# Kernel optimization log

Hardware: AMD Instinct MI355X
Metric: run time of the kernel (lower is better)

Reference implementation:

```python
import jax, jax.numpy as jnp
import numpy as np

EPS = 1e-5
B, S, P = 2, 512, 4096
TD, SD, H, ED = 512, 384, 8, 32
HD = TD // H


def _ln(x, g, b):
    m = jnp.mean(x, axis=-1, keepdims=True)
    v = jnp.var(x, axis=-1, keepdims=True)
    return (x - m) * jax.lax.rsqrt(v + EPS) * g + b


def setup_inputs() -> dict:
    key = jax.random.key(0)
    ks = iter(jax.random.split(key, 24))

    def lin(din, dout):
        W = jax.random.normal(next(ks), (din, dout), jnp.float32) / np.sqrt(din)
        b = jnp.zeros((dout,), jnp.float32)
        return W, b

    Wq, bq = lin(TD, TD)
    Wk, bk = lin(SD, TD)
    Wv, bv = lin(SD, TD)
    Wo, bo = lin(TD, TD)
    W1, b1 = lin(TD, 4 * TD)
    W2, b2 = lin(4 * TD, TD)
    edge_emb = jax.random.normal(next(ks), (H, ED), jnp.float32)
    ep_w = jax.random.normal(next(ks), (ED,), jnp.float32) / np.sqrt(ED)
    ep_b = jnp.zeros((), jnp.float32)

    return dict(
        text_features=jax.random.normal(next(ks), (B, S, TD), jnp.float32),
        shape_features=jax.random.normal(next(ks), (B, P, SD), jnp.float32),
        tn_g=jnp.ones((TD,), jnp.float32), tn_b=jnp.zeros((TD,), jnp.float32),
        sn_g=jnp.ones((SD,), jnp.float32), sn_b=jnp.zeros((SD,), jnp.float32),
        Wq=Wq, bq=bq, Wk=Wk, bk=bk, Wv=Wv, bv=bv,
        edge_emb=edge_emb, ep_w=ep_w, ep_b=ep_b,
        Wo=Wo, bo=bo,
        on_g=jnp.ones((TD,), jnp.float32), on_b=jnp.zeros((TD,), jnp.float32),
        W1=W1, b1=b1, W2=W2, b2=b2,
        fn_g=jnp.ones((TD,), jnp.float32), fn_b=jnp.zeros((TD,), jnp.float32),
    )


def reference(text_features, shape_features, tn_g, tn_b, sn_g, sn_b,
              Wq, bq, Wk, bk, Wv, bv, edge_emb, ep_w, ep_b, Wo, bo,
              on_g, on_b, W1, b1, W2, b2, fn_g, fn_b):
    b, n, _ = text_features.shape
    tn = _ln(text_features, tn_g, tn_b)
    sn = _ln(shape_features, sn_g, sn_b)
    residual = text_features

    # [b, h, n, d] projections
    q = (tn @ Wq + bq).reshape(b, n, H, HD).transpose(0, 2, 1, 3)
    k = (sn @ Wk + bk).reshape(b, -1, H, HD).transpose(0, 2, 1, 3)
    v = (sn @ Wv + bv).reshape(b, -1, H, HD).transpose(0, 2, 1, 3)

    scale = HD ** -0.5
    base_attn = jnp.einsum('bhid,bhjd->bhij', q, k) * scale  # [b,h,n,p]

    # edge_attn[:,h] = base_attn[:,h,:,:,None] * edge_emb[h]; then Linear(ED,1)+LeakyReLU.
    # Algebraically: score = leaky_relu(base_attn * (edge_emb @ ep_w) + ep_b)
    s = edge_emb @ ep_w  # [H] per-head scalar
    edge_scores = jax.nn.leaky_relu(base_attn * s[None, :, None, None] + ep_b, 0.2)

    attn = jax.nn.softmax(base_attn + edge_scores, axis=-1)
    out = jnp.einsum('bhij,bhjd->bhid', attn, v)
    out = out.transpose(0, 2, 1, 3).reshape(b, n, TD)
    out = out @ Wo + bo
    out = _ln(residual + out, on_g, on_b)

    ffn = jax.nn.gelu(out @ W1 + b1, approximate=False) @ W2 + b2
    out = _ln(out + ffn, fn_g, fn_b)
    return out, attn
```

## Files before the change

kernel.cpp:

```cpp
#include <hip/hip_runtime.h>
#include <math.h>

#define B_  2
#define S_  512
#define P_  4096
#define TD_ 512
#define SD_ 384
#define H_  8
#define HD_ 64
#define FF_ 2048

typedef _Float16 half8 __attribute__((ext_vector_type(8)));
typedef _Float16 half4 __attribute__((ext_vector_type(4)));
typedef float floatx4 __attribute__((ext_vector_type(4)));

__device__ __forceinline__ half8 f4x2_to_h8(float4 a, float4 b) {
    half8 r;
    r[0] = (_Float16)a.x; r[1] = (_Float16)a.y; r[2] = (_Float16)a.z; r[3] = (_Float16)a.w;
    r[4] = (_Float16)b.x; r[5] = (_Float16)b.y; r[6] = (_Float16)b.z; r[7] = (_Float16)b.w;
    return r;
}

__device__ __forceinline__ float2 block_sum2(float a, float b) {
    for (int off = 32; off > 0; off >>= 1) {
        a += __shfl_down(a, off);
        b += __shfl_down(b, off);
    }
    __shared__ float sa[8], sb[8];
    int w = threadIdx.x >> 6;
    if ((threadIdx.x & 63) == 0) { sa[w] = a; sb[w] = b; }
    __syncthreads();
    int nw = blockDim.x >> 6;
    float ta = 0.f, tb = 0.f;
    for (int i = 0; i < nw; ++i) { ta += sa[i]; tb += sb[i]; }
    __syncthreads();
    return make_float2(ta, tb);
}

__global__ __launch_bounds__(256) void prep_kernel(
    const float* __restrict__ s0p, const float* __restrict__ s1p,
    const float* __restrict__ s2p, const float* __restrict__ s3p,
    const float* __restrict__ s4p, const float* __restrict__ s5p,
    _Float16* __restrict__ d0p, _Float16* __restrict__ d1p,
    _Float16* __restrict__ d2p, _Float16* __restrict__ d3p,
    _Float16* __restrict__ d4p, _Float16* __restrict__ d5p,
    const float* __restrict__ text, const float* __restrict__ shape,
    const float* __restrict__ tn_g, const float* __restrict__ tn_b,
    const float* __restrict__ sn_g, const float* __restrict__ sn_b,
    _Float16* __restrict__ tn_h, _Float16* __restrict__ sn_h,
    float* __restrict__ ctx_zero)
{
    __shared__ float ts[32][33];
    int id = blockIdx.x;
    int tid = threadIdx.x;
    if (id < 2944) {
        const float* src; _Float16* dst; int K, N, t, nlog;
        if (id < 256)       { src=s0p; dst=d0p; K=512;  N=512;  t=id;       nlog=4; }
        else if (id < 448)  { src=s1p; dst=d1p; K=384;  N=512;  t=id-256;   nlog=4; }
        else if (id < 640)  { src=s2p; dst=d2p; K=384;  N=512;  t=id-448;   nlog=4; }
        else if (id < 896)  { src=s3p; dst=d3p; K=512;  N=512;  t=id-640;   nlog=4; }
        else if (id < 1920) { src=s4p; dst=d4p; K=512;  N=2048; t=id-896;   nlog=6; }
        else                { src=s5p; dst=d5p; K=2048; N=512;  t=id-1920;  nlog=4; }
        int n0 = (t & ((1 << nlog) - 1)) << 5;
        int k0 = (t >> nlog) << 5;
#pragma unroll
        for (int i = 0; i < 4; ++i) {
            int e = i * 256 + tid;
            int kk = e >> 5, nn = e & 31;
            ts[kk][nn] = src[(size_t)(k0 + kk) * N + n0 + nn];
        }
        __syncthreads();
#pragma unroll
        for (int i = 0; i < 4; ++i) {
            int e = i * 256 + tid;
            int nn = e >> 5, kk = e & 31;
            dst[(size_t)(n0 + nn) * K + k0 + kk] = (_Float16)ts[kk][nn];
        }
        return;
    }
    if (id >= 12160) {
        int i = (id - 12160) * 256 + tid;
        ((float4*)ctx_zero)[i] = make_float4(0.f, 0.f, 0.f, 0.f);
        return;
    }
    int row = id - 2944;
    const float* xr; const float* g; const float* be; _Float16* yr; int D;
    if (row < 1024) {
        D = 512; xr = text + (size_t)row * 512; g = tn_g; be = tn_b;
        yr = tn_h + (size_t)row * 512;
    } else {
        int r2 = row - 1024;
        D = 384; xr = shape + (size_t)r2 * 384; g = sn_g; be = sn_b;
        yr = sn_h + (size_t)r2 * 384;
    }
    float s = 0.f, s2 = 0.f;
    for (int i = tid; i < D; i += 256) {
        float v = xr[i]; s += v; s2 += v * v;
    }
    float2 r = block_sum2(s, s2);
    float mean = r.x / (float)D;
    float var  = r.y / (float)D - mean * mean;
    float rstd = rsqrtf(var + 1e-5f);
    for (int i = tid; i < D; i += 256)
        yr[i] = (_Float16)((xr[i] - mean) * rstd * g[i] + be[i]);
}

__global__ __launch_bounds__(256) void ln_add_kernel(
    const float* __restrict__ a, const float* __restrict__ c, int np, int cstride,
    const float* __restrict__ g, const float* __restrict__ be,
    float* __restrict__ yf, _Float16* __restrict__ yh)
{
    int row = blockIdx.x;
    int i0 = threadIdx.x, i1 = threadIdx.x + 256;
    const float* ar = a + (size_t)row * 512;
    const float* cr = c + (size_t)row * 512;
    float v0 = ar[i0], v1 = ar[i1];
    for (int t = 0; t < np; ++t) {
        v0 += cr[(size_t)t * cstride + i0];
        v1 += cr[(size_t)t * cstride + i1];
    }
    float2 rd = block_sum2(v0 + v1, v0 * v0 + v1 * v1);
    float mean = rd.x / 512.f;
    float var  = rd.y / 512.f - mean * mean;
    float rstd = rsqrtf(var + 1e-5f);
    float o0 = (v0 - mean) * rstd * g[i0] + be[i0];
    float o1 = (v1 - mean) * rstd * g[i1] + be[i1];
    if (yf) { yf[(size_t)row * 512 + i0] = o0; yf[(size_t)row * 512 + i1] = o1; }
    if (yh) { yh[(size_t)row * 512 + i0] = (_Float16)o0; yh[(size_t)row * 512 + i1] = (_Float16)o1; }
}

template<int ACT, int OUTF, int OUTH, int SPLITK, int AF32>
__global__ __launch_bounds__(256) void gemm_f16_kernel(
    const _Float16* __restrict__ A, const _Float16* __restrict__ Bt,
    const float* __restrict__ bias, float* __restrict__ Cf,
    _Float16* __restrict__ Ch, int M, int N, int K)
{
    __shared__ _Float16 As[128 * 40];
    __shared__ _Float16 Bs[128 * 40];
    int tid = threadIdx.x;
    int bm = blockIdx.y * 128, bn = blockIdx.x * 128;
    int wave = tid >> 6, lane = tid & 63, quad = lane >> 4, r = lane & 15;
    int mh = (wave & 1) * 64, nh = (wave >> 1) * 64;

    floatx4 acc[4][4];
    floatx4 zz = {0.f, 0.f, 0.f, 0.f};
#pragma unroll
    for (int i = 0; i < 4; ++i)
#pragma unroll
        for (int j = 0; j < 4; ++j) acc[i][j] = zz;

    int srow = tid >> 2;
    int sko  = (tid & 3) * 8;

    int ksplit = (SPLITK > 1) ? blockIdx.z : 0;
    int kbeg = ksplit * (K / SPLITK);
    int kend = kbeg + K / SPLITK;

    const float*    Af  = (const float*)A;
    const _Float16* Ap0 = A  + (size_t)(bm + srow) * K + sko;
    const _Float16* Ap1 = A  + (size_t)(bm + srow + 64) * K + sko;
    const float*    Af0 = Af + (size_t)(bm + srow) * K + sko;
    const float*    Af1 = Af + (size_t)(bm + srow + 64) * K + sko;
    const _Float16* Bp0 = Bt + (size_t)(bn + srow) * K + sko;
    const _Float16* Bp1 = Bt + (size_t)(bn + srow + 64) * K + sko;

    half8 ra0, ra1;
    float4 fa0l, fa0h, fa1l, fa1h;
    if (AF32) {
        fa0l = *(const float4*)(Af0 + kbeg); fa0h = *(const float4*)(Af0 + kbeg + 4);
        fa1l = *(const float4*)(Af1 + kbeg); fa1h = *(const float4*)(Af1 + kbeg + 4);
    } else {
        ra0 = *(const half8*)(Ap0 + kbeg);
        ra1 = *(const half8*)(Ap1 + kbeg);
    }
    half8 rb0 = *(const half8*)(Bp0 + kbeg);
    half8 rb1 = *(const half8*)(Bp1 + kbeg);

    for (int k0 = kbeg; k0 < kend; k0 += 32) {
        if (AF32) {
            *(half8*)&As[srow * 40 + sko]        = f4x2_to_h8(fa0l, fa0h);
            *(half8*)&As[(srow + 64) * 40 + sko] = f4x2_to_h8(fa1l, fa1h);
        } else {
            *(half8*)&As[srow * 40 + sko]        = ra0;
            *(half8*)&As[(srow + 64) * 40 + sko] = ra1;
        }
        *(half8*)&Bs[srow * 40 + sko]        = rb0;
        *(half8*)&Bs[(srow + 64) * 40 + sko] = rb1;
        __syncthreads();
        if (k0 + 32 < kend) {
            if (AF32) {
                fa0l = *(const float4*)(Af0 + k0 + 32); fa0h = *(const float4*)(Af0 + k0 + 36);
                fa1l = *(const float4*)(Af1 + k0 + 32); fa1h = *(const float4*)(Af1 + k0 + 36);
            } else {
                ra0 = *(const half8*)(Ap0 + k0 + 32);
                ra1 = *(const half8*)(Ap1 + k0 + 32);
            }
            rb0 = *(const half8*)(Bp0 + k0 + 32);
            rb1 = *(const half8*)(Bp1 + k0 + 32);
        }
        half8 af[4], bf[4];
#pragma unroll
        for (int t = 0; t < 4; ++t) {
            af[t] = *(const half8*)&As[(mh + t * 16 + r) * 40 + quad * 8];
            bf[t] = *(const half8*)&Bs[(nh + t * 16 + r) * 40 + quad * 8];
        }
#pragma unroll
        for (int i = 0; i < 4; ++i)
#pragma unroll
            for (int j = 0; j < 4; ++j)
                acc[i][j] = __builtin_amdgcn_mfma_f32_16x16x32_f16(af[i], bf[j], acc[i][j], 0, 0, 0);
        __syncthreads();
    }

#pragma unroll
    for (int j = 0; j < 4; ++j) {
        int col = bn + nh + j * 16 + r;
        float bv = (SPLITK == 1 || ksplit == 0) ? bias[col] : 0.f;
#pragma unroll
        for (int i = 0; i < 4; ++i) {
#pragma unroll
            for (int g = 0; g < 4; ++g) {
                int row = bm + mh + i * 16 + quad * 4 + g;
                float v = acc[i][j][g] + bv;
                if (ACT) v = 0.5f * v * (1.0f + erff(v * 0.70710678118654752f));
                if (OUTF) Cf[(size_t)ksplit * M * N + (size_t)row * N + col] = v;
                if (OUTH) Ch[(size_t)row * N + col] = (_Float16)v;
            }
        }
    }
}

__global__ __launch_bounds__(512) void qkv_gemm_kernel(
    const _Float16* __restrict__ tn, const _Float16* __restrict__ sn,
    const _Float16* __restrict__ Wqt, const _Float16* __restrict__ Wkt,
    const _Float16* __restrict__ Wvt,
    const float* __restrict__ bq, const float* __restrict__ bk,
    const float* __restrict__ bv,
    _Float16* __restrict__ Qh, _Float16* __restrict__ Kh, _Float16* __restrict__ Vth)
{
    __shared__ _Float16 As[256 * 40];
    __shared__ _Float16 Bs[128 * 40];
    int by = blockIdx.y;
    const _Float16* A; const _Float16* Bt; const float* bias; _Float16* out;
    int K, bm, vt;
    if (by < 4)       { A = tn; Bt = Wqt; bias = bq; K = 512; bm = by * 256;        vt = 0; out = Qh;  }
    else if (by < 36) { A = sn; Bt = Wkt; bias = bk; K = 384; bm = (by - 4) * 256;  vt = 0; out = Kh;  }
    else              { A = sn; Bt = Wvt; bias = bv; K = 384; bm = (by - 36) * 256; vt = 1; out = Vth; }
    int bn = blockIdx.x * 128;
    int tid = threadIdx.x;
    int wave = tid >> 6, lane = tid & 63, quad = lane >> 4, r = lane & 15;
    int mh = (wave >> 1) * 64, nh = (wave & 1) * 64;

    floatx4 acc[4][4];
    floatx4 zz = {0.f, 0.f, 0.f, 0.f};
#pragma unroll
    for (int i = 0; i < 4; ++i)
#pragma unroll
        for (int j = 0; j < 4; ++j) acc[i][j] = zz;

    int arow = tid >> 2, ako = (tid & 3) * 8;
    const _Float16* ApA0 = A  + (size_t)(bm + arow) * K + ako;
    const _Float16* ApA1 = A  + (size_t)(bm + arow + 128) * K + ako;
    const _Float16* BpB  = Bt + (size_t)(bn + arow) * K + ako;

    half8 ra0 = *(const half8*)(ApA0);
    half8 ra1 = *(const half8*)(ApA1);
    half8 rb  = *(const half8*)(BpB);

    for (int k0 = 0; k0 < K; k0 += 32) {
        *(half8*)&As[arow * 40 + ako]         = ra0;
        *(half8*)&As[(arow + 128) * 40 + ako] = ra1;
        *(half8*)&Bs[arow * 40 + ako]         = rb;
        __syncthreads();
        if (k0 + 32 < K) {
            ra0 = *(const half8*)(ApA0 + k0 + 32);
            ra1 = *(const half8*)(ApA1 + k0 + 32);
            rb  = *(const half8*)(BpB  + k0 + 32);
        }
        half8 af[4], bf[4];
#pragma unroll
        for (int t = 0; t < 4; ++t) {
            af[t] = *(const half8*)&As[(mh + t * 16 + r) * 40 + quad * 8];
            bf[t] = *(const half8*)&Bs[(nh + t * 16 + r) * 40 + quad * 8];
        }
#pragma unroll
        for (int i = 0; i < 4; ++i)
#pragma unroll
            for (int j = 0; j < 4; ++j)
                acc[i][j] = __builtin_amdgcn_mfma_f32_16x16x32_f16(af[i], bf[j], acc[i][j], 0, 0, 0);
        __syncthreads();
    }

#pragma unroll
    for (int j = 0; j < 4; ++j) {
        int col = bn + nh + j * 16 + r;
        float bvv = bias[col];
#pragma unroll
        for (int i = 0; i < 4; ++i) {
#pragma unroll
            for (int g = 0; g < 4; ++g) {
                int row = bm + mh + i * 16 + quad * 4 + g;
                float v = acc[i][j][g] + bvv;
                if (!vt) {
                    out[(size_t)row * 512 + col] = (_Float16)v;
                } else {
                    int bb = row >> 12, pp = row & 4095;
                    int hh = col >> 6,  dd = col & 63;
                    out[((size_t)((bb * 8 + hh) * 64 + dd)) * 4096 + pp] = (_Float16)v;
                }
            }
        }
    }
}

__global__ __launch_bounds__(256) void score_stats_kernel(
    const _Float16* __restrict__ Qh, const _Float16* __restrict__ Kh,
    const float* __restrict__ edge_emb, const float* __restrict__ ep_w,
    const float* __restrict__ ep_b, float2* __restrict__ part)
{
    __shared__ _Float16 Qs[128 * 72];
    __shared__ _Float16 Ks[128 * 72];
    __shared__ float mred[2][128];
    __shared__ float sred[2][128];
    int bid = blockIdx.x;
    int slot = bid & 7, idx = bid >> 3;
    int g4 = slot + 8 * (idx >> 2);
    int s0 = (idx & 3) * 128;
    int p0 = (g4 & 31) * 128;
    int bh = g4 >> 5, h = bh & 7, b = bh >> 3;
    int tid = threadIdx.x;
    int wave = tid >> 6, lane = tid & 63, quad = lane >> 4, r = lane & 15;
    int mh = (wave & 1) * 64, nh = (wave >> 1) * 64;

#pragma unroll
    for (int i = 0; i < 4; ++i) {
        int row = i * 32 + (tid >> 3);
        int ko  = (tid & 7) * 8;
        *(half8*)&Qs[row * 72 + ko] = *(const half8*)(Qh + (size_t)(b * S_ + s0 + row) * TD_ + h * HD_ + ko);
        *(half8*)&Ks[row * 72 + ko] = *(const half8*)(Kh + (size_t)(b * P_ + p0 + row) * TD_ + h * HD_ + ko);
    }
    float s_h = 0.f;
#pragma unroll
    for (int e = 0; e < 32; ++e) s_h += edge_emb[h * 32 + e] * ep_w[e];
    float epbv = ep_b[0];
    __syncthreads();

    floatx4 acc[4][4];
    floatx4 zz = {0.f, 0.f, 0.f, 0.f};
#pragma unroll
    for (int i = 0; i < 4; ++i)
#pragma unroll
        for (int j = 0; j < 4; ++j) acc[i][j] = zz;

#pragma unroll
    for (int c = 0; c < 2; ++c) {
        half8 af[4], bf[4];
#pragma unroll
        for (int t = 0; t < 4; ++t) {
            af[t] = *(const half8*)&Qs[(mh + t * 16 + r) * 72 + c * 32 + quad * 8];
            bf[t] = *(const half8*)&Ks[(nh + t * 16 + r) * 72 + c * 32 + quad * 8];
        }
#pragma unroll
        for (int i = 0; i < 4; ++i)
#pragma unroll
            for (int j = 0; j < 4; ++j)
                acc[i][j] = __builtin_amdgcn_mfma_f32_16x16x32_f16(af[i], bf[j], acc[i][j], 0, 0, 0);
    }

    const float scale = 0.125f;
#pragma unroll
    for (int i = 0; i < 4; ++i)
#pragma unroll
        for (int j = 0; j < 4; ++j)
#pragma unroll
            for (int g = 0; g < 4; ++g) {
                float base = acc[i][j][g] * scale;
                float t = fmaf(base, s_h, epbv);
                float e = (t >= 0.f) ? t : 0.2f * t;
                acc[i][j][g] = base + e;
            }

    float mv[16], sv[16];
#pragma unroll
    for (int i = 0; i < 4; ++i)
#pragma unroll
        for (int g = 0; g < 4; ++g)
            mv[i * 4 + g] = fmaxf(fmaxf(acc[i][0][g], acc[i][1][g]),
                                  fmaxf(acc[i][2][g], acc[i][3][g]));
#pragma unroll
    for (int mask = 1; mask <= 8; mask <<= 1)
#pragma unroll
        for (int t = 0; t < 16; ++t)
            mv[t] = fmaxf(mv[t], __shfl_xor(mv[t], mask));
#pragma unroll
    for (int i = 0; i < 4; ++i)
#pragma unroll
        for (int g = 0; g < 4; ++g) {
            float s = 0.f;
#pragma unroll
            for (int j = 0; j < 4; ++j) s += __expf(acc[i][j][g] - mv[i * 4 + g]);
            sv[i * 4 + g] = s;
        }
#pragma unroll
    for (int mask = 1; mask <= 8; mask <<= 1)
#pragma unroll
        for (int t = 0; t < 16; ++t)
            sv[t] += __shfl_xor(sv[t], mask);

    if (r == 0) {
#pragma unroll
        for (int i = 0; i < 4; ++i)
#pragma unroll
            for (int g = 0; g < 4; ++g) {
                int row = mh + i * 16 + quad * 4 + g;
                mred[wave >> 1][row] = mv[i * 4 + g];
                sred[wave >> 1][row] = sv[i * 4 + g];
            }
    }
    __syncthreads();
    if (tid < 128) {
        float m0 = mred[0][tid], m1 = mred[1][tid];
        float m = fmaxf(m0, m1);
        float s = sred[0][tid] * __expf(m0 - m) + sred[1][tid] * __expf(m1 - m);
        part[(size_t)(p0 >> 7) * (B_ * H_ * S_) + (size_t)bh * S_ + s0 + tid] = make_float2(m, s);
    }
}

__global__ __launch_bounds__(256) void attn_pv_kernel(
    const _Float16* __restrict__ Qh, const _Float16* __restrict__ Kh,
    const _Float16* __restrict__ Vt,
    const float* __restrict__ edge_emb, const float* __restrict__ ep_w,
    const float* __restrict__ ep_b, const float2* __restrict__ part,
    float* __restrict__ attn, float* __restrict__ ctx_f32)
{
    __shared__ _Float16 Qs[32 * 72];
    __shared__ _Float16 Ks[128 * 72];
    __shared__ _Float16 Vs[64 * 136];
    __shared__ _Float16 As[32 * 136];
    __shared__ float2 ms_sh[32];

    int bid = blockIdx.x;
    int slot = bid & 7, idx = bid >> 3;
    int g16 = slot + 8 * (idx >> 4);
    int s0 = (idx & 15) * 32;
    int split = g16 & 7;
    int bh = g16 >> 3, h = bh & 7, b = bh >> 3;
    int tid = threadIdx.x;
    int wave = tid >> 6, lane = tid & 63, quad = lane >> 4, r = lane & 15;

    {
        int row = tid >> 3, ko = (tid & 7) * 8;
        *(half8*)&Qs[row * 72 + ko] =
            *(const half8*)(Qh + (size_t)(b * S_ + s0 + row) * TD_ + h * HD_ + ko);
    }
    if (tid < 32) {
        int base = bh * S_ + s0 + tid;
        float2 v = part[base];
        float m = v.x, l = v.y;
#pragma unroll
        for (int t = 1; t < 32; ++t) {
            float2 p = part[(size_t)t * (B_ * H_ * S_) + base];
            float nm = fmaxf(m, p.x);
            l = l * __expf(m - nm) + p.y * __expf(p.x - nm);
            m = nm;
        }
        ms_sh[tid] = make_float2(m, 1.0f / l);
    }

    float s_h = 0.f;
#pragma unroll
    for (int e = 0; e < 32; ++e) s_h += edge_emb[h * 32 + e] * ep_w[e];
    float epbv = ep_b[0];

    const _Float16* Kbase = Kh + (size_t)b * P_ * TD_ + h * HD_;
    const _Float16* Vbase = Vt + (size_t)bh * 64 * P_;

    int pg0 = split * 512;
    half8 rk[4], rv[4];
#pragma unroll
    for (int ii = 0; ii < 4; ++ii) {
        int e = ii * 256 + tid;
        rk[ii] = *(const half8*)(Kbase + (size_t)(pg0 + (e >> 3)) * TD_ + (e & 7) * 8);
        rv[ii] = *(const half8*)(Vbase + (size_t)(e >> 4) * P_ + pg0 + (e & 15) * 8);
    }

    floatx4 zz = {0.f, 0.f, 0.f, 0.f};
    floatx4 accpv[2];
    accpv[0] = zz; accpv[1] = zz;
    const float scale = 0.125f;

    for (int c = 0; c < 4; ++c) {
        int pg = pg0 + c * 128;
#pragma unroll
        for (int ii = 0; ii < 4; ++ii) {
            int e = ii * 256 + tid;
            *(half8*)&Ks[(e >> 3) * 72 + (e & 7) * 8]  = rk[ii];
            *(half8*)&Vs[(e >> 4) * 136 + (e & 15) * 8] = rv[ii];
        }
        __syncthreads();
        if (c < 3) {
            int pn = pg + 128;
#pragma unroll
            for (int ii = 0; ii < 4; ++ii) {
                int e = ii * 256 + tid;
                rk[ii] = *(const half8*)(Kbase + (size_t)(pn + (e >> 3)) * TD_ + (e & 7) * 8);
                rv[ii] = *(const half8*)(Vbase + (size_t)(e >> 4) * P_ + pn + (e & 15) * 8);
            }
        }

        floatx4 accs[2][2];
        accs[0][0] = zz; accs[0][1] = zz; accs[1][0] = zz; accs[1][1] = zz;
#pragma unroll
        for (int c2 = 0; c2 < 2; ++c2) {
            half8 aq[2], bk2[2];
#pragma unroll
            for (int i = 0; i < 2; ++i)
                aq[i] = *(const half8*)&Qs[(i * 16 + r) * 72 + c2 * 32 + quad * 8];
#pragma unroll
            for (int j = 0; j < 2; ++j)
                bk2[j] = *(const half8*)&Ks[(wave * 32 + j * 16 + r) * 72 + c2 * 32 + quad * 8];
#pragma unroll
            for (int i = 0; i < 2; ++i)
#pragma unroll
                for (int j = 0; j < 2; ++j)
                    accs[i][j] = __builtin_amdgcn_mfma_f32_16x16x32_f16(aq[i], bk2[j], accs[i][j], 0, 0, 0);
        }

#pragma unroll
        for (int i = 0; i < 2; ++i)
#pragma unroll
            for (int j = 0; j < 2; ++j) {
                int colp = wave * 32 + j * 16 + r;
#pragma unroll
                for (int g = 0; g < 4; ++g) {
                    int srow = i * 16 + quad * 4 + g;
                    float base = accs[i][j][g] * scale;
                    float t = fmaf(base, s_h, epbv);
                    float e = (t >= 0.f) ? t : 0.2f * t;
                    float z = base + e;
                    float2 ms = ms_sh[srow];
                    float p = __expf(z - ms.x) * ms.y;
                    As[srow * 136 + colp] = (_Float16)p;
                }
            }
        __syncthreads();

#pragma unroll
        for (int it = 0; it < 4; ++it) {
            int e = it * 256 + tid;
            int row = e >> 5, c4 = (e & 31) * 4;
            half4 hv = *(const half4*)&As[row * 136 + c4];
            floatx4 fv = { (float)hv[0], (float)hv[1], (float)hv[2], (float)hv[3] };
            __builtin_nontemporal_store(fv,
                (floatx4*)&attn[((size_t)bh * S_ + s0 + row) * P_ + pg + c4]);
        }

#pragma unroll
        for (int cc = 0; cc < 4; ++cc) {
            half8 bv = *(const half8*)&Vs[(wave * 16 + r) * 136 + cc * 32 + quad * 8];
#pragma unroll
            for (int i2 = 0; i2 < 2; ++i2) {
                half8 ap = *(const half8*)&As[(i2 * 16 + r) * 136 + cc * 32 + quad * 8];
                accpv[i2] = __builtin_amdgcn_mfma_f32_16x16x32_f16(ap, bv, accpv[i2], 0, 0, 0);
            }
        }
        __syncthreads();
    }

#pragma unroll
    for (int i2 = 0; i2 < 2; ++i2)
#pragma unroll
        for (int g = 0; g < 4; ++g) {
            int srow = s0 + i2 * 16 + quad * 4 + g;
            int d = wave * 16 + r;
            atomicAdd(&ctx_f32[(size_t)(b * S_ + srow) * TD_ + h * HD_ + d], accpv[i2][g]);
        }
}

extern "C" void kernel_launch(void* const* d_in, const int* in_sizes, int n_in,
                              void* d_out, int out_size, void* d_ws, size_t ws_size,
                              hipStream_t stream) {
    const float* text  = (const float*)d_in[0];
    const float* shape = (const float*)d_in[1];
    const float* tn_g  = (const float*)d_in[2];
    const float* tn_b  = (const float*)d_in[3];
    const float* sn_g  = (const float*)d_in[4];
    const float* sn_b  = (const float*)d_in[5];
    const float* Wq    = (const float*)d_in[6];
    const float* bq    = (const float*)d_in[7];
    const float* Wk    = (const float*)d_in[8];
    const float* bk    = (const float*)d_in[9];
    const float* Wv    = (const float*)d_in[10];
    const float* bv    = (const float*)d_in[11];
    const float* edge  = (const float*)d_in[12];
    const float* epw   = (const float*)d_in[13];
    const float* epb   = (const float*)d_in[14];
    const float* Wo    = (const float*)d_in[15];
    const float* bo    = (const float*)d_in[16];
    const float* on_g  = (const float*)d_in[17];
    const float* on_b  = (const float*)d_in[18];
    const float* W1    = (const float*)d_in[19];
    const float* b1    = (const float*)d_in[20];
    const float* W2    = (const float*)d_in[21];
    const float* b2    = (const float*)d_in[22];
    const float* fn_g  = (const float*)d_in[23];
    const float* fn_b  = (const float*)d_in[24];

    float* out_f  = (float*)d_out;
    float* attn_f = out_f + (size_t)B_ * S_ * TD_;

    char* w = (char*)d_ws;
    _Float16* tn_h   = (_Float16*)w; w += (size_t)1024 * 512 * 2;
    _Float16* sn_h   = (_Float16*)w; w += (size_t)8192 * 384 * 2;
    _Float16* Q_h    = (_Float16*)w; w += (size_t)1024 * 512 * 2;
    _Float16* K_h    = (_Float16*)w; w += (size_t)8192 * 512 * 2;
    _Float16* Vt_h   = (_Float16*)w; w += (size_t)16 * 64 * 4096 * 2;
    float*    ctx_f32 = (float*)w;   w += (size_t)1024 * 512 * 4;
    _Float16* out1_h = (_Float16*)w; w += (size_t)1024 * 512 * 2;
    _Float16* h1_h   = (_Float16*)w; w += (size_t)1024 * 2048 * 2;
    _Float16* Wqt    = (_Float16*)w; w += (size_t)512 * 512 * 2;
    _Float16* Wkt    = (_Float16*)w; w += (size_t)512 * 384 * 2;
    _Float16* Wvt    = (_Float16*)w; w += (size_t)512 * 384 * 2;
    _Float16* Wot    = (_Float16*)w; w += (size_t)512 * 512 * 2;
    _Float16* W1t    = (_Float16*)w; w += (size_t)2048 * 512 * 2;
    _Float16* W2t    = (_Float16*)w; w += (size_t)512 * 2048 * 2;
    float*    out1_f = (float*)w;    w += (size_t)1024 * 512 * 4;
    float*    ctx_part = (float*)w;  w += (size_t)4 * 1024 * 512 * 4;

    float2* part = (float2*)sn_h;

    prep_kernel<<<2944 + 1024 + 8192 + 512, 256, 0, stream>>>(
        Wq, Wk, Wv, Wo, W1, W2, Wqt, Wkt, Wvt, Wot, W1t, W2t,
        text, shape, tn_g, tn_b, sn_g, sn_b, tn_h, sn_h, ctx_f32);

    qkv_gemm_kernel<<<dim3(4, 68), 512, 0, stream>>>(tn_h, sn_h, Wqt, Wkt, Wvt,
                                                     bq, bk, bv, Q_h, K_h, Vt_h);

    score_stats_kernel<<<2048, 256, 0, stream>>>(Q_h, K_h, edge, epw, epb, part);
    attn_pv_kernel<<<2048, 256, 0, stream>>>(Q_h, K_h, Vt_h, edge, epw, epb, part, attn_f, ctx_f32);

    gemm_f16_kernel<0,1,0,4,1><<<dim3(4, 8, 4), 256, 0, stream>>>(
        (const _Float16*)ctx_f32, Wot, bo, ctx_part, nullptr, 1024, 512, 512);
    ln_add_kernel<<<B_ * S_, 256, 0, stream>>>(text, ctx_part, 4, 1024 * 512, on_g, on_b, out1_f, out1_h);

    gemm_f16_kernel<1,0,1,1,0><<<dim3(16, 8), 256, 0, stream>>>(out1_h, W1t, b1, nullptr, h1_h, 1024, 2048, 512);
    gemm_f16_kernel<0,1,0,4,0><<<dim3(4, 8, 4), 256, 0, stream>>>(h1_h, W2t, b2, ctx_part, nullptr, 1024, 512, 2048);
    ln_add_kernel<<<B_ * S_, 256, 0, stream>>>(out1_f, ctx_part, 4, 1024 * 512, fn_g, fn_b, out_f, nullptr);
}
```

Before: 335.2 us.

## Cache per-tile softmax numerators in fp16 buffer instead of recomputing QK scores

The stats pass now writes exp(score - tile max) as fp16 into a large workspace buffer, and a new PV kernel reads it back, rescales it by the combined softmax statistics, writes attn and does the PV MFMA. This drops the second QK^T recomputation in the attention kernel. The cost is an extra 64MB fp16 write and read. The path runs only if the workspace is large enough, otherwise the old recompute path is kept. Storing probabilities in fp16 before rescaling adds some precision loss to the attn output.

Result: slower. 366.5 us (+9.3%).

```diff
diff --git a/kernel.cpp b/kernel.cpp
--- a/kernel.cpp
+++ b/kernel.cpp
@@ -313,15 +313,20 @@
     }
 }
 
+template<int WP>
 __global__ __launch_bounds__(256) void score_stats_kernel(
     const _Float16* __restrict__ Qh, const _Float16* __restrict__ Kh,
     const float* __restrict__ edge_emb, const float* __restrict__ ep_w,
-    const float* __restrict__ ep_b, float2* __restrict__ part)
+    const float* __restrict__ ep_b, float2* __restrict__ part,
+    _Float16* __restrict__ Pbuf)
 {
-    __shared__ _Float16 Qs[128 * 72];
-    __shared__ _Float16 Ks[128 * 72];
+    __shared__ _Float16 smem[2 * 128 * 72];
     __shared__ float mred[2][128];
     __shared__ float sred[2][128];
+    _Float16* Qs = smem;
+    _Float16* Ks = smem + 128 * 72;
+    _Float16* Ps = smem;
+
     int bid = blockIdx.x;
     int slot = bid & 7, idx = bid >> 3;
     int g4 = slot + 8 * (idx >> 2);
@@ -398,7 +403,11 @@
         for (int g = 0; g < 4; ++g) {
             float s = 0.f;
 #pragma unroll
-            for (int j = 0; j < 4; ++j) s += __expf(acc[i][j][g] - mv[i * 4 + g]);
+            for (int j = 0; j < 4; ++j) {
+                float e = __expf(acc[i][j][g] - mv[i * 4 + g]);
+                acc[i][j][g] = e;
+                s += e;
+            }
             sv[i * 4 + g] = s;
         }
 #pragma unroll
@@ -418,15 +427,157 @@
             }
     }
     __syncthreads();
+
+    if (WP) {
+#pragma unroll
+        for (int i = 0; i < 4; ++i)
+#pragma unroll
+            for (int g = 0; g < 4; ++g) {
+                int row = mh + i * 16 + quad * 4 + g;
+                float mfull = fmaxf(mred[0][row], mred[1][row]);
+                float sc = __expf(mv[i * 4 + g] - mfull);
+#pragma unroll
+                for (int j = 0; j < 4; ++j)
+                    Ps[row * 136 + (nh + j * 16 + r)] = (_Float16)(acc[i][j][g] * sc);
+            }
+    }
+
     if (tid < 128) {
         float m0 = mred[0][tid], m1 = mred[1][tid];
         float m = fmaxf(m0, m1);
         float s = sred[0][tid] * __expf(m0 - m) + sred[1][tid] * __expf(m1 - m);
         part[(size_t)(p0 >> 7) * (B_ * H_ * S_) + (size_t)bh * S_ + s0 + tid] = make_float2(m, s);
     }
-}
-
-__global__ __launch_bounds__(256) void attn_pv_kernel(
+
+    if (WP) {
+        __syncthreads();
+#pragma unroll
+        for (int it = 0; it < 8; ++it) {
+            int e = it * 256 + tid;
+            int row = e >> 4, c8 = (e & 15) * 8;
+            half8 hv = *(const half8*)&Ps[row * 136 + c8];
+            __builtin_nontemporal_store(hv,
+                (half8*)(Pbuf + ((size_t)bh * S_ + s0 + row) * P_ + p0 + c8));
+        }
+    }
+}
+
+__global__ __launch_bounds__(256) void attn_pv_pc_kernel(
+    const _Float16* __restrict__ Pbuf, const _Float16* __restrict__ Vt,
+    const float2* __restrict__ part,
+    float* __restrict__ attn, float* __restrict__ ctx_f32)
+{
+    __shared__ _Float16 Vs[64 * 136];
+    __shared__ _Float16 As[32 * 136];
+    __shared__ float rs_sh[4][32];
+
+    int bid = blockIdx.x;
+    int slot = bid & 7, idx = bid >> 3;
+    int g16 = slot + 8 * (idx >> 4);
+    int s0 = (idx & 15) * 32;
+    int split = g16 & 7;
+    int bh = g16 >> 3, h = bh & 7, b = bh >> 3;
+    int tid = threadIdx.x;
+    int wave = tid >> 6, lane = tid & 63, quad = lane >> 4, r = lane & 15;
+
+    if (tid < 32) {
+        int base = bh * S_ + s0 + tid;
+        float2 v = part[base];
+        float m = v.x, l = v.y;
+#pragma unroll
+        for (int t = 1; t < 32; ++t) {
+            float2 p = part[(size_t)t * (B_ * H_ * S_) + base];
+            float nm = fmaxf(m, p.x);
+            l = l * __expf(m - nm) + p.y * __expf(p.x - nm);
+            m = nm;
+        }
+        float invl = 1.0f / l;
+#pragma unroll
+        for (int c = 0; c < 4; ++c) {
+            float mt = part[(size_t)(split * 4 + c) * (B_ * H_ * S_) + base].x;
+            rs_sh[c][tid] = __expf(mt - m) * invl;
+        }
+    }
+
+    const _Float16* Vbase = Vt + (size_t)bh * 64 * P_;
+    const _Float16* Pb    = Pbuf + ((size_t)bh * S_ + s0) * P_;
+    int pg0 = split * 512;
+    int prow = tid >> 4, ppo = (tid & 15) * 8;
+
+    half8 rv[4], rp0, rp1;
+#pragma unroll
+    for (int ii = 0; ii < 4; ++ii) {
+        int e = ii * 256 + tid;
+        rv[ii] = *(const half8*)(Vbase + (size_t)(e >> 4) * P_ + pg0 + (e & 15) * 8);
+    }
+    rp0 = *(const half8*)(Pb + (size_t)prow * P_ + pg0 + ppo);
+    rp1 = *(const half8*)(Pb + (size_t)(prow + 16) * P_ + pg0 + ppo);
+
+    floatx4 zz = {0.f, 0.f, 0.f, 0.f};
+    floatx4 accpv[2];
+    accpv[0] = zz; accpv[1] = zz;
+
+    __syncthreads();
+
+    for (int c = 0; c < 4; ++c) {
+        int pg = pg0 + c * 128;
+#pragma unroll
+        for (int ii = 0; ii < 4; ++ii) {
+            int e = ii * 256 + tid;
+            *(half8*)&Vs[(e >> 4) * 136 + (e & 15) * 8] = rv[ii];
+        }
+        float rs0 = rs_sh[c][prow], rs1 = rs_sh[c][prow + 16];
+        half8 a0, a1;
+        floatx4 f0a, f0b, f1a, f1b;
+#pragma unroll
+        for (int k = 0; k < 4; ++k) {
+            float u0 = (float)rp0[k]     * rs0; f0a[k] = u0; a0[k]     = (_Float16)u0;
+            float u1 = (float)rp0[k + 4] * rs0; f0b[k] = u1; a0[k + 4] = (_Float16)u1;
+            float w0 = (float)rp1[k]     * rs1; f1a[k] = w0; a1[k]     = (_Float16)w0;
+            float w1 = (float)rp1[k + 4] * rs1; f1b[k] = w1; a1[k + 4] = (_Float16)w1;
+        }
+        *(half8*)&As[prow * 136 + ppo]        = a0;
+        *(half8*)&As[(prow + 16) * 136 + ppo] = a1;
+        float* ar0 = &attn[((size_t)bh * S_ + s0 + prow) * P_ + pg + ppo];
+        float* ar1 = &attn[((size_t)bh * S_ + s0 + prow + 16) * P_ + pg + ppo];
+        __builtin_nontemporal_store(f0a, (floatx4*)ar0);
+        __builtin_nontemporal_store(f0b, (floatx4*)(ar0 + 4));
+        __builtin_nontemporal_store(f1a, (floatx4*)ar1);
+        __builtin_nontemporal_store(f1b, (floatx4*)(ar1 + 4));
+        __syncthreads();
+        if (c < 3) {
+            int pn = pg + 128;
+#pragma unroll
+            for (int ii = 0; ii < 4; ++ii) {
+                int e = ii * 256 + tid;
+                rv[ii] = *(const half8*)(Vbase + (size_t)(e >> 4) * P_ + pn + (e & 15) * 8);
+            }
+            rp0 = *(const half8*)(Pb + (size_t)prow * P_ + pn + ppo);
+            rp1 = *(const half8*)(Pb + (size_t)(prow + 16) * P_ + pn + ppo);
+        }
+#pragma unroll
+        for (int cc = 0; cc < 4; ++cc) {
+            half8 bv = *(const half8*)&Vs[(wave * 16 + r) * 136 + cc * 32 + quad * 8];
+#pragma unroll
+            for (int i2 = 0; i2 < 2; ++i2) {
+                half8 ap = *(const half8*)&As[(i2 * 16 + r) * 136 + cc * 32 + quad * 8];
+                accpv[i2] = __builtin_amdgcn_mfma_f32_16x16x32_f16(ap, bv, accpv[i2], 0, 0, 0);
+            }
+        }
+        __syncthreads();
+    }
+
+#pragma unroll
+    for (int i2 = 0; i2 < 2; ++i2)
+#pragma unroll
+        for (int g = 0; g < 4; ++g) {
+            int srow = s0 + i2 * 16 + quad * 4 + g;
+            int d = wave * 16 + r;
+            atomicAdd(&ctx_f32[(size_t)(b * S_ + srow) * TD_ + h * HD_ + d], accpv[i2][g]);
+        }
+}
+
+__global__ __launch_bounds__(256) void attn_pv_rc_kernel(
     const _Float16* __restrict__ Qh, const _Float16* __restrict__ Kh,
     const _Float16* __restrict__ Vt,
     const float* __restrict__ edge_emb, const float* __restrict__ ep_w,
@@ -624,8 +775,13 @@
     _Float16* Wot    = (_Float16*)w; w += (size_t)512 * 512 * 2;
     _Float16* W1t    = (_Float16*)w; w += (size_t)2048 * 512 * 2;
     _Float16* W2t    = (_Float16*)w; w += (size_t)512 * 2048 * 2;
-    float*    out1_f = (float*)w;    w += (size_t)1024 * 512 * 4;
-    float*    ctx_part = (float*)w;  w += (size_t)4 * 1024 * 512 * 4;
+    char* region = w;
+    float*    out1_f   = (float*)region;
+    float*    ctx_part = (float*)(region + (size_t)1024 * 512 * 4);
+    _Float16* P_buf    = (_Float16*)region;
+    size_t fixed = (size_t)(region - (char*)d_ws);
+    size_t need_pc = fixed + (size_t)8192 * 4096 * 2;
+    bool pc = ws_size >= need_pc;
 
     float2* part = (float2*)sn_h;
 
@@ -636,8 +792,13 @@
     qkv_gemm_kernel<<<dim3(4, 68), 512, 0, stream>>>(tn_h, sn_h, Wqt, Wkt, Wvt,
                                                      bq, bk, bv, Q_h, K_h, Vt_h);
 
-    score_stats_kernel<<<2048, 256, 0, stream>>>(Q_h, K_h, edge, epw, epb, part);
-    attn_pv_kernel<<<2048, 256, 0, stream>>>(Q_h, K_h, Vt_h, edge, epw, epb, part, attn_f, ctx_f32);
+    if (pc) {
+        score_stats_kernel<1><<<2048, 256, 0, stream>>>(Q_h, K_h, edge, epw, epb, part, P_buf);
+        attn_pv_pc_kernel<<<2048, 256, 0, stream>>>(P_buf, Vt_h, part, attn_f, ctx_f32);
+    } else {
+        score_stats_kernel<0><<<2048, 256, 0, stream>>>(Q_h, K_h, edge, epw, epb, part, nullptr);
+        attn_pv_rc_kernel<<<2048, 256, 0, stream>>>(Q_h, K_h, Vt_h, edge, epw, epb, part, attn_f, ctx_f32);
+    }
 
     gemm_f16_kernel<0,1,0,4,1><<<dim3(4, 8, 4), 256, 0, stream>>>(
         (const _Float16*)ctx_f32, Wot, bo, ctx_part, nullptr, 1024, 512, 512);
```
